# Optimization experiments

Measured on AMD Instinct MI355X. Metric: run time of the kernel, lower is better.

## Reference

```python
import jax, jax.numpy as jnp
import numpy as np

EPS = 1e-5  # torch LayerNorm default


def setup_inputs() -> dict:
    key = jax.random.key(0)
    ks = jax.random.split(key, 4)
    B, S, D = 8, 1024, 768
    return {
        "q": jax.random.normal(ks[0], (B, S, D), dtype=jnp.float32),
        "k": jax.random.normal(ks[1], (B, S, D), dtype=jnp.float32),
        "v": jax.random.normal(ks[2], (B, S, D), dtype=jnp.float32),
        "W": jax.random.normal(ks[3], (D, D), dtype=jnp.float32) * (1.0 / np.sqrt(D)),
        "gamma": jnp.ones((D,), dtype=jnp.float32),
        "beta": jnp.zeros((D,), dtype=jnp.float32),
        "n_heads": 12,
    }


def reference(q, k, v, W, gamma, beta, n_heads):
    # Shapes: q,k,v [B,S,D]; W [D,D] (torch Linear weight, y = x @ W.T)
    B, S, D = q.shape
    Dh = D // n_heads

    proj = lambda x: jax.nn.relu(x @ W.T)
    q1, k1, v1 = proj(q), proj(k), proj(v)

    # chunk(dim=2) + cat(dim=0) == reshape to per-head [B,S,H,Dh]
    split = lambda x: x.reshape(B, S, n_heads, Dh)
    qh, kh, vh = split(q1), split(k1), split(v1)

    scale = 1.0 / (Dh ** 0.5)
    scores = jnp.einsum("bqhd,bkhd->bhqk", qh, kh) * scale  # [B,H,S,S]
    attn = jax.nn.softmax(scores, axis=-1)  # dropout is identity in eval mode
    out = jnp.einsum("bhqk,bkhd->bqhd", attn, vh).reshape(B, S, D)

    # `outputs += outputs + q` in torch -> outputs = 2*outputs + q
    out = 2.0 * out + q

    mu = jnp.mean(out, axis=-1, keepdims=True)
    var = jnp.var(out, axis=-1, keepdims=True)
    return (out - mu) / jnp.sqrt(var + EPS) * gamma + beta
```

## Files before the change

### kernel.cpp

```cpp
#include <hip/hip_runtime.h>
#include <hip/hip_bf16.h>

#define B_  8
#define S_  1024
#define D_  768
#define H_  12
#define DH_ 64

typedef __attribute__((ext_vector_type(8))) short bf16x8;
typedef __attribute__((ext_vector_type(4))) float f32x4;
typedef __attribute__((ext_vector_type(16))) float f32x16;

__device__ inline short f2bf(float f) {
    unsigned u = __builtin_bit_cast(unsigned, f);
    u = (u + 0x7fffu + ((u >> 16) & 1u)) >> 16;
    return (short)u;
}
__device__ inline float exp2_fast(float x) {
    float r; asm("v_exp_f32 %0, %1" : "=v"(r) : "v"(x)); return r;
}
__device__ inline unsigned cvt_pk_bf16(float lo, float hi) {
    unsigned r; asm("v_cvt_pk_bf16_f32 %0, %1, %2" : "=v"(r) : "v"(lo), "v"(hi)); return r;
}
__device__ inline float rcp_fast(float x) {
    float r; asm("v_rcp_f32 %0, %1" : "=v"(r) : "v"(x)); return r;
}
__device__ inline void plswap(unsigned& a, unsigned& b) {
    auto r = __builtin_amdgcn_permlane32_swap(a, b, false, false);
    a = r[0]; b = r[1];
}
__device__ inline float2 xhalves(float x) {
    unsigned u = __builtin_bit_cast(unsigned, x);
    auto r = __builtin_amdgcn_permlane32_swap(u, u, false, false);
    return make_float2(__builtin_bit_cast(float, r[0]),
                       __builtin_bit_cast(float, r[1]));
}

__global__ __launch_bounds__(256) void proj_kernel(
    const float* __restrict__ q, const float* __restrict__ k,
    const float* __restrict__ v, const float* __restrict__ W,
    short* __restrict__ q1, short* __restrict__ k1, short* __restrict__ v1t)
{
    __shared__ __align__(16) char lds_raw[32768];

    int p  = blockIdx.x;
    int L  = (p & 7) * 144 + (p >> 3);
    int mt = L / 6, nt = L % 6;
    int t  = mt >> 6;
    int m0 = (mt & 63) << 7;
    int n0 = nt << 7;
    const float* X = (t == 0) ? q : (t == 1) ? k : v;

    int tid = threadIdx.x, lane = tid & 63, w = tid >> 6;
    int wr = w >> 1, wc = w & 1;
    int l15 = lane & 15, g = lane >> 4;

    int srow = tid >> 1, h = tid & 1;
    const float* ax = X + (size_t)(m0 + srow) * D_ + h * 16;
    const float* bx = W + (size_t)(n0 + srow) * D_ + h * 16;

    int wb0 = srow * 64 + ((((h << 1) | 0) ^ (srow & 3)) << 4);
    int wb1 = srow * 64 + ((((h << 1) | 1) ^ (srow & 3)) << 4);
    int fs = (g ^ (l15 & 3)) << 4;

    f32x4 la[4], lb[4];
#define LOADAB(step) do { int _c = (step) * 32; \
        la[0] = *(const f32x4*)(ax + _c);      la[1] = *(const f32x4*)(ax + _c + 4); \
        la[2] = *(const f32x4*)(ax + _c + 8);  la[3] = *(const f32x4*)(ax + _c + 12); \
        lb[0] = *(const f32x4*)(bx + _c);      lb[1] = *(const f32x4*)(bx + _c + 4); \
        lb[2] = *(const f32x4*)(bx + _c + 8);  lb[3] = *(const f32x4*)(bx + _c + 12); \
    } while (0)
#define CONVW(bufbase) do { \
        uint4 ua0, ua1, ub0, ub1; \
        ua0.x = cvt_pk_bf16(la[0][0], la[0][1]); ua0.y = cvt_pk_bf16(la[0][2], la[0][3]); \
        ua0.z = cvt_pk_bf16(la[1][0], la[1][1]); ua0.w = cvt_pk_bf16(la[1][2], la[1][3]); \
        ua1.x = cvt_pk_bf16(la[2][0], la[2][1]); ua1.y = cvt_pk_bf16(la[2][2], la[2][3]); \
        ua1.z = cvt_pk_bf16(la[3][0], la[3][1]); ua1.w = cvt_pk_bf16(la[3][2], la[3][3]); \
        ub0.x = cvt_pk_bf16(lb[0][0], lb[0][1]); ub0.y = cvt_pk_bf16(lb[0][2], lb[0][3]); \
        ub0.z = cvt_pk_bf16(lb[1][0], lb[1][1]); ub0.w = cvt_pk_bf16(lb[1][2], lb[1][3]); \
        ub1.x = cvt_pk_bf16(lb[2][0], lb[2][1]); ub1.y = cvt_pk_bf16(lb[2][2], lb[2][3]); \
        ub1.z = cvt_pk_bf16(lb[3][0], lb[3][1]); ub1.w = cvt_pk_bf16(lb[3][2], lb[3][3]); \
        *(uint4*)(lds_raw + (bufbase) + wb0)        = ua0; \
        *(uint4*)(lds_raw + (bufbase) + wb1)        = ua1; \
        *(uint4*)(lds_raw + (bufbase) + 8192 + wb0) = ub0; \
        *(uint4*)(lds_raw + (bufbase) + 8192 + wb1) = ub1; \
    } while (0)

    f32x4 acc[4][4];
    #pragma unroll
    for (int m = 0; m < 4; m++)
        #pragma unroll
        for (int n = 0; n < 4; n++) acc[m][n] = (f32x4){0.f, 0.f, 0.f, 0.f};

    LOADAB(0);
    CONVW(0);
    LOADAB(1);
    asm volatile("s_waitcnt lgkmcnt(0)" ::: "memory");
    __builtin_amdgcn_s_barrier();
    asm volatile("" ::: "memory");

    #pragma unroll 2
    for (int s = 0; s < 24; ++s) {
        if (s < 23) CONVW(((s + 1) & 1) << 14);
        if (s < 22) LOADAB(s + 2);
        const char* bufp = lds_raw + ((s & 1) << 14);
        bf16x8 af[4], bfv[4];
        #pragma unroll
        for (int m = 0; m < 4; m++)
            af[m] = *(const bf16x8*)(bufp + (wr * 64 + m * 16 + l15) * 64 + fs);
        #pragma unroll
        for (int n = 0; n < 4; n++)
            bfv[n] = *(const bf16x8*)(bufp + 8192 + (wc * 64 + n * 16 + l15) * 64 + fs);
        __builtin_amdgcn_s_setprio(1);
        #pragma unroll
        for (int m = 0; m < 4; m++)
            #pragma unroll
            for (int n = 0; n < 4; n++)
                acc[m][n] = __builtin_amdgcn_mfma_f32_16x16x32_bf16(
                    af[m], bfv[n], acc[m][n], 0, 0, 0);
        __builtin_amdgcn_s_setprio(0);
        if (s < 23) {
            asm volatile("s_waitcnt lgkmcnt(0)" ::: "memory");
            __builtin_amdgcn_s_barrier();
            asm volatile("" ::: "memory");
        }
    }
#undef LOADAB
#undef CONVW

    __syncthreads();
    const float sc1 = (t == 1) ? 0.18033688011112793f : 1.0f;
    #pragma unroll
    for (int m = 0; m < 4; m++) {
        int rb = wr * 64 + m * 16 + (g << 2);
        #pragma unroll
        for (int n = 0; n < 4; n++) {
            int cb = wc * 64 + n * 16 + l15;
            #pragma unroll
            for (int r = 0; r < 4; r++) {
                short vv = f2bf(fmaxf(acc[m][n][r], 0.f) * sc1);
                int rr = (t == 2) ? cb : rb + r;
                int cc = (t == 2) ? rb + r : cb;
                *(short*)(lds_raw + rr * 256 + (((cc >> 3) ^ (rr & 15)) << 4)
                          + ((cc & 7) << 1)) = vv;
            }
        }
    }
    __syncthreads();
    int row = tid >> 1;
    int c0  = (tid & 1) << 6;
    bf16x8 ov[8];
    #pragma unroll
    for (int j = 0; j < 8; j++)
        ov[j] = *(const bf16x8*)(lds_raw + row * 256 +
                 ((((c0 >> 3) + j) ^ (row & 15)) << 4));
    if (t == 2) {
        int gc = n0 + row;
        int hh2 = gc >> 6, dh = gc & 63;
        int bb = m0 >> 10, s0 = m0 & 1023;
        short* dst = v1t + (((size_t)bb * H_ + hh2) * DH_ + dh) * S_ + s0 + c0;
        #pragma unroll
        for (int j = 0; j < 8; j++) *(bf16x8*)(dst + j * 8) = ov[j];
    } else {
        int m = m0 + row;
        int bb = m >> 10, ss = m & 1023;
        int hh2 = (n0 >> 6) + (tid & 1);
        short* dst = (t ? k1 : q1) + (((size_t)bb * H_ + hh2) * S_ + ss) * DH_;
        #pragma unroll
        for (int j = 0; j < 8; j++) *(bf16x8*)(dst + j * 8) = ov[j];
    }
}

__global__ __launch_bounds__(256, 3) void attn_kernel(
    const short* __restrict__ q1, const short* __restrict__ k1,
    const short* __restrict__ v1t, float* __restrict__ out)
{
    __shared__ short Klds[2][4096];
    __shared__ short Vlds[2][4096];
    __shared__ float lsum_lds[4][32];

    int d    = blockIdx.x;
    int head = (d & 7) + ((d >> 6) << 3);
    int qi   = (d >> 3) & 7;
    int bb   = head / H_, hh = head % H_;

    int tid = threadIdx.x, lane = tid & 63, w = tid >> 6;
    int l31 = lane & 31, hi = lane >> 5;
    int qbase = (qi * 4 + w) * 32;

    const short* Qp = q1  + (size_t)head * S_ * DH_;
    const short* Kp = k1  + (size_t)head * S_ * DH_;
    const short* Vp = v1t + (size_t)head * DH_ * S_;

    int sr = tid >> 2, sc = tid & 3;
    int swz0 = sr * 128 + ((sc       ^ (sr & 7)) << 4);
    int swz1 = sr * 128 + (((sc + 4) ^ (sr & 7)) << 4);

    bf16x8 stK0, stK1, stV0, stV1;

#define LOADST(kvb) do { \
        const short* _kg = Kp + (size_t)((kvb) + sr) * DH_; \
        const short* _vg = Vp + (size_t)sr * S_ + (kvb); \
        stK0 = *(const bf16x8*)(_kg + sc * 8); \
        stK1 = *(const bf16x8*)(_kg + (sc + 4) * 8); \
        stV0 = *(const bf16x8*)(_vg + sc * 8); \
        stV1 = *(const bf16x8*)(_vg + (sc + 4) * 8); \
    } while (0)
#define WRITEST(buf) do { \
        char* _kb = (char*)&Klds[buf][0]; \
        char* _vb = (char*)&Vlds[buf][0]; \
        *(bf16x8*)(_kb + swz0) = stK0; \
        *(bf16x8*)(_kb + swz1) = stK1; \
        *(bf16x8*)(_vb + swz0) = stV0; \
        *(bf16x8*)(_vb + swz1) = stV1; \
    } while (0)

    bf16x8 qf[4];
    #pragma unroll
    for (int kb = 0; kb < 4; kb++)
        qf[kb] = *(const bf16x8*)(Qp + (size_t)(qbase + l31) * DH_ + kb * 16 + hi * 8);

    f32x16 o0, o1;
    #pragma unroll
    for (int r = 0; r < 16; r++) { o0[r] = 0.f; o1[r] = 0.f; }
    float mreg = -1e30f, lsum = 0.f;

    int xk = l31 & 7;

    auto subtile = [&](int cur, int j) {
        const char* Kt = (const char*)&Klds[cur][0];
        const char* Vt = (const char*)&Vlds[cur][0];
        int rK = (32 * j + l31) * 128;
        bf16x8 kf0 = *(const bf16x8*)(Kt + rK + (((0 + hi) ^ xk) << 4));
        bf16x8 kf1 = *(const bf16x8*)(Kt + rK + (((2 + hi) ^ xk) << 4));
        bf16x8 kf2 = *(const bf16x8*)(Kt + rK + (((4 + hi) ^ xk) << 4));
        bf16x8 kf3 = *(const bf16x8*)(Kt + rK + (((6 + hi) ^ xk) << 4));
        int rV0 = l31 * 128, rV1 = (32 + l31) * 128;
        int s0 = ((4 * j + hi) ^ xk) << 4, s1 = ((4 * j + 2 + hi) ^ xk) << 4;
        bf16x8 vf00 = *(const bf16x8*)(Vt + rV0 + s0);
        bf16x8 vf01 = *(const bf16x8*)(Vt + rV0 + s1);
        bf16x8 vf10 = *(const bf16x8*)(Vt + rV1 + s0);
        bf16x8 vf11 = *(const bf16x8*)(Vt + rV1 + s1);

        f32x16 s;
        #pragma unroll
        for (int r = 0; r < 16; r++) s[r] = 0.f;
        __builtin_amdgcn_s_setprio(1);
        s = __builtin_amdgcn_mfma_f32_32x32x16_bf16(kf0, qf[0], s, 0, 0, 0);
        s = __builtin_amdgcn_mfma_f32_32x32x16_bf16(kf1, qf[1], s, 0, 0, 0);
        s = __builtin_amdgcn_mfma_f32_32x32x16_bf16(kf2, qf[2], s, 0, 0, 0);
        s = __builtin_amdgcn_mfma_f32_32x32x16_bf16(kf3, qf[3], s, 0, 0, 0);
        __builtin_amdgcn_s_setprio(0);

        float t0 = fmaxf(s[0], s[1]),   t1 = fmaxf(s[2], s[3]);
        float t2 = fmaxf(s[4], s[5]),   t3 = fmaxf(s[6], s[7]);
        float t4 = fmaxf(s[8], s[9]),   t5 = fmaxf(s[10], s[11]);
        float t6 = fmaxf(s[12], s[13]), t7 = fmaxf(s[14], s[15]);
        float u0 = fmaxf(t0, t1), u1 = fmaxf(t2, t3);
        float u2 = fmaxf(t4, t5), u3 = fmaxf(t6, t7);
        float pmax = fmaxf(fmaxf(u0, u1), fmaxf(u2, u3));
        float2 ph = xhalves(pmax);
        pmax = fmaxf(ph.x, ph.y);

        if (!__all(pmax <= mreg + 8.f)) {
            float mn = fmaxf(mreg, pmax);
            float sc_ = exp2_fast(mreg - mn);
            mreg = mn; lsum *= sc_;
            if (hi == 0) lsum_lds[w][l31] = sc_;
            asm volatile("s_waitcnt lgkmcnt(0)" ::: "memory");
            #pragma unroll
            for (int r = 0; r < 16; r++) {
                int crow = (r & 3) + ((r >> 2) << 3) + (hi << 2);
                float srw = lsum_lds[w][crow];
                o0[r] *= srw; o1[r] *= srw;
            }
        }

        #pragma unroll
        for (int r = 0; r < 16; r++) s[r] = exp2_fast(s[r] - mreg);

        float a0 = s[0] + s[1],   a1 = s[2] + s[3];
        float a2 = s[4] + s[5],   a3 = s[6] + s[7];
        float a4 = s[8] + s[9],   a5 = s[10] + s[11];
        float a6 = s[12] + s[13], a7 = s[14] + s[15];
        float rsum = ((a0 + a1) + (a2 + a3)) + ((a4 + a5) + (a6 + a7));
        float2 rh = xhalves(rsum);
        lsum += rh.x + rh.y;

        unsigned c0 = cvt_pk_bf16(s[0], s[1]);
        unsigned c1 = cvt_pk_bf16(s[2], s[3]);
        unsigned c2 = cvt_pk_bf16(s[4], s[5]);
        unsigned c3 = cvt_pk_bf16(s[6], s[7]);
        unsigned c4 = cvt_pk_bf16(s[8], s[9]);
        unsigned c5 = cvt_pk_bf16(s[10], s[11]);
        unsigned c6 = cvt_pk_bf16(s[12], s[13]);
        unsigned c7 = cvt_pk_bf16(s[14], s[15]);
        plswap(c0, c2);
        plswap(c1, c3);
        plswap(c4, c6);
        plswap(c5, c7);

        union U { unsigned u[4]; bf16x8 v; };
        U f0, f1;
        f0.u[0] = c0; f0.u[1] = c1; f0.u[2] = c2; f0.u[3] = c3;
        f1.u[0] = c4; f1.u[1] = c5; f1.u[2] = c6; f1.u[3] = c7;

        __builtin_amdgcn_s_setprio(1);
        o0 = __builtin_amdgcn_mfma_f32_32x32x16_bf16(f0.v, vf00, o0, 0, 0, 0);
        o0 = __builtin_amdgcn_mfma_f32_32x32x16_bf16(f1.v, vf01, o0, 0, 0, 0);
        o1 = __builtin_amdgcn_mfma_f32_32x32x16_bf16(f0.v, vf10, o1, 0, 0, 0);
        o1 = __builtin_amdgcn_mfma_f32_32x32x16_bf16(f1.v, vf11, o1, 0, 0, 0);
        __builtin_amdgcn_s_setprio(0);
    };

    LOADST(0);
    WRITEST(0);
    LOADST(64);
    asm volatile("s_waitcnt lgkmcnt(0)" ::: "memory");
    __builtin_amdgcn_s_barrier();
    asm volatile("" ::: "memory");

    int cur = 0;
    for (int t = 0; t < 16; t++) {
        if (t < 15) {
            WRITEST(cur ^ 1);
            if (t < 14) LOADST((t + 2) * 64);
        }
        subtile(cur, 0);
        subtile(cur, 1);
        if (t < 15) {
            asm volatile("" ::: "memory");
            asm volatile("s_waitcnt lgkmcnt(0)" ::: "memory");
            __builtin_amdgcn_s_barrier();
            asm volatile("" ::: "memory");
        }
        cur ^= 1;
    }
#undef LOADST
#undef WRITEST

    if (hi == 0) lsum_lds[w][l31] = lsum;
    asm volatile("s_waitcnt lgkmcnt(0)" ::: "memory");
    #pragma unroll
    for (int r = 0; r < 16; r++) {
        int crow = (r & 3) + ((r >> 2) << 3) + (hi << 2);
        float inv = rcp_fast(lsum_lds[w][crow]);
        float* op = out + ((size_t)(bb * S_ + qbase + crow)) * D_ + hh * DH_ + l31;
        op[0]  = o0[r] * inv;
        op[32] = o1[r] * inv;
    }
}

__global__ __launch_bounds__(192) void ln_kernel(
    const float* __restrict__ qin, const float* __restrict__ gamma,
    const float* __restrict__ beta, float* __restrict__ out)
{
    int row = blockIdx.x;
    int tid = threadIdx.x;
    size_t base = (size_t)row * D_ + tid * 4;

    f32x4 o  = *(const f32x4*)(out + base);
    f32x4 qv = *(const f32x4*)(qin + base);
    f32x4 x;
    float sum = 0.f, sq = 0.f;
    #pragma unroll
    for (int i = 0; i < 4; i++) {
        x[i] = 2.f * o[i] + qv[i];
        sum += x[i];
        sq  += x[i] * x[i];
    }
    #pragma unroll
    for (int msk = 1; msk < 64; msk <<= 1) {
        sum += __shfl_xor(sum, msk);
        sq  += __shfl_xor(sq, msk);
    }
    __shared__ float s1[3], s2[3];
    if ((tid & 63) == 0) { s1[tid >> 6] = sum; s2[tid >> 6] = sq; }
    __syncthreads();
    sum = s1[0] + s1[1] + s1[2];
    sq  = s2[0] + s2[1] + s2[2];
    float mu   = sum * (1.f / D_);
    float var  = sq * (1.f / D_) - mu * mu;
    float rstd = rsqrtf(var + 1e-5f);
    f32x4 g = *(const f32x4*)(gamma + tid * 4);
    f32x4 b = *(const f32x4*)(beta + tid * 4);
    f32x4 y;
    #pragma unroll
    for (int i = 0; i < 4; i++)
        y[i] = (x[i] - mu) * rstd * g[i] + b[i];
    *(f32x4*)(out + base) = y;
}

extern "C" void kernel_launch(void* const* d_in, const int* in_sizes, int n_in,
                              void* d_out, int out_size, void* d_ws, size_t ws_size,
                              hipStream_t stream)
{
    const float* q     = (const float*)d_in[0];
    const float* k     = (const float*)d_in[1];
    const float* v     = (const float*)d_in[2];
    const float* W     = (const float*)d_in[3];
    const float* gamma = (const float*)d_in[4];
    const float* beta  = (const float*)d_in[5];

    size_t per = (size_t)B_ * H_ * S_ * DH_;
    short* q1  = (short*)d_ws;
    short* k1  = q1 + per;
    short* v1t = k1 + per;
    float* out = (float*)d_out;

    proj_kernel<<<dim3(1152), dim3(256), 0, stream>>>(q, k, v, W, q1, k1, v1t);
    attn_kernel<<<dim3(768), dim3(256), 0, stream>>>(q1, k1, v1t, out);
    ln_kernel<<<dim3(B_ * S_), dim3(192), 0, stream>>>(q, gamma, beta, out);
}
```

Measured before the change: 130.2 us.

## Load projection GEMM tiles directly into LDS with global_load_lds

Result: no change. 128.0 us (-1.7%).

```diff
diff --git a/kernel.cpp b/kernel.cpp
--- a/kernel.cpp
+++ b/kernel.cpp
@@ -34,6 +34,12 @@
     auto r = __builtin_amdgcn_permlane32_swap(u, u, false, false);
     return make_float2(__builtin_bit_cast(float, r[0]),
                        __builtin_bit_cast(float, r[1]));
+}
+__device__ inline void gl_lds16(const float* gsrc, char* ldst) {
+    __builtin_amdgcn_global_load_lds(
+        (const __attribute__((address_space(1))) unsigned int*)gsrc,
+        (__attribute__((address_space(3))) unsigned int*)ldst,
+        16, 0, 0);
 }
 
 __global__ __launch_bounds__(256) void proj_kernel(
@@ -55,36 +61,15 @@
     int wr = w >> 1, wc = w & 1;
     int l15 = lane & 15, g = lane >> 4;
 
-    int srow = tid >> 1, h = tid & 1;
-    const float* ax = X + (size_t)(m0 + srow) * D_ + h * 16;
-    const float* bx = W + (size_t)(n0 + srow) * D_ + h * 16;
-
-    int wb0 = srow * 64 + ((((h << 1) | 0) ^ (srow & 3)) << 4);
-    int wb1 = srow * 64 + ((((h << 1) | 1) ^ (srow & 3)) << 4);
-    int fs = (g ^ (l15 & 3)) << 4;
-
-    f32x4 la[4], lb[4];
-#define LOADAB(step) do { int _c = (step) * 32; \
-        la[0] = *(const f32x4*)(ax + _c);      la[1] = *(const f32x4*)(ax + _c + 4); \
-        la[2] = *(const f32x4*)(ax + _c + 8);  la[3] = *(const f32x4*)(ax + _c + 12); \
-        lb[0] = *(const f32x4*)(bx + _c);      lb[1] = *(const f32x4*)(bx + _c + 4); \
-        lb[2] = *(const f32x4*)(bx + _c + 8);  lb[3] = *(const f32x4*)(bx + _c + 12); \
-    } while (0)
-#define CONVW(bufbase) do { \
-        uint4 ua0, ua1, ub0, ub1; \
-        ua0.x = cvt_pk_bf16(la[0][0], la[0][1]); ua0.y = cvt_pk_bf16(la[0][2], la[0][3]); \
-        ua0.z = cvt_pk_bf16(la[1][0], la[1][1]); ua0.w = cvt_pk_bf16(la[1][2], la[1][3]); \
-        ua1.x = cvt_pk_bf16(la[2][0], la[2][1]); ua1.y = cvt_pk_bf16(la[2][2], la[2][3]); \
-        ua1.z = cvt_pk_bf16(la[3][0], la[3][1]); ua1.w = cvt_pk_bf16(la[3][2], la[3][3]); \
-        ub0.x = cvt_pk_bf16(lb[0][0], lb[0][1]); ub0.y = cvt_pk_bf16(lb[0][2], lb[0][3]); \
-        ub0.z = cvt_pk_bf16(lb[1][0], lb[1][1]); ub0.w = cvt_pk_bf16(lb[1][2], lb[1][3]); \
-        ub1.x = cvt_pk_bf16(lb[2][0], lb[2][1]); ub1.y = cvt_pk_bf16(lb[2][2], lb[2][3]); \
-        ub1.z = cvt_pk_bf16(lb[3][0], lb[3][1]); ub1.w = cvt_pk_bf16(lb[3][2], lb[3][3]); \
-        *(uint4*)(lds_raw + (bufbase) + wb0)        = ua0; \
-        *(uint4*)(lds_raw + (bufbase) + wb1)        = ua1; \
-        *(uint4*)(lds_raw + (bufbase) + 8192 + wb0) = ub0; \
-        *(uint4*)(lds_raw + (bufbase) + 8192 + wb1) = ub1; \
-    } while (0)
+    const float* srcA[4];
+    const float* srcB[4];
+    #pragma unroll
+    for (int i = 0; i < 4; i++) {
+        int r  = w * 32 + i * 8 + (lane >> 3);
+        int sp = (lane & 7) ^ (r & 7);
+        srcA[i] = X + (size_t)(m0 + r) * D_ + sp * 4;
+        srcB[i] = W + (size_t)(n0 + r) * D_ + sp * 4;
+    }
 
     f32x4 acc[4][4];
     #pragma unroll
@@ -92,25 +77,41 @@
         #pragma unroll
         for (int n = 0; n < 4; n++) acc[m][n] = (f32x4){0.f, 0.f, 0.f, 0.f};
 
-    LOADAB(0);
-    CONVW(0);
-    LOADAB(1);
-    asm volatile("s_waitcnt lgkmcnt(0)" ::: "memory");
-    __builtin_amdgcn_s_barrier();
-    asm volatile("" ::: "memory");
-
-    #pragma unroll 2
-    for (int s = 0; s < 24; ++s) {
-        if (s < 23) CONVW(((s + 1) & 1) << 14);
-        if (s < 22) LOADAB(s + 2);
-        const char* bufp = lds_raw + ((s & 1) << 14);
+    for (int kb = 0; kb < 24; ++kb) {
+        __builtin_amdgcn_s_barrier();
+        asm volatile("" ::: "memory");
+        #pragma unroll
+        for (int i = 0; i < 4; i++) {
+            gl_lds16(srcA[i] + kb * 32, lds_raw + w * 4096 + i * 1024);
+            gl_lds16(srcB[i] + kb * 32, lds_raw + 16384 + w * 4096 + i * 1024);
+        }
+        asm volatile("s_waitcnt vmcnt(0)" ::: "memory");
+        __builtin_amdgcn_s_barrier();
+        asm volatile("" ::: "memory");
+
         bf16x8 af[4], bfv[4];
         #pragma unroll
-        for (int m = 0; m < 4; m++)
-            af[m] = *(const bf16x8*)(bufp + (wr * 64 + m * 16 + l15) * 64 + fs);
-        #pragma unroll
-        for (int n = 0; n < 4; n++)
-            bfv[n] = *(const bf16x8*)(bufp + 8192 + (wc * 64 + n * 16 + l15) * 64 + fs);
+        for (int m = 0; m < 4; m++) {
+            int r = wr * 64 + m * 16 + l15;
+            const char* rp = lds_raw + r * 128;
+            f32x4 lo = *(const f32x4*)(rp + (((2 * g)     ^ (r & 7)) << 4));
+            f32x4 hi = *(const f32x4*)(rp + (((2 * g + 1) ^ (r & 7)) << 4));
+            uint4 pk;
+            pk.x = cvt_pk_bf16(lo[0], lo[1]); pk.y = cvt_pk_bf16(lo[2], lo[3]);
+            pk.z = cvt_pk_bf16(hi[0], hi[1]); pk.w = cvt_pk_bf16(hi[2], hi[3]);
+            af[m] = __builtin_bit_cast(bf16x8, pk);
+        }
+        #pragma unroll
+        for (int n = 0; n < 4; n++) {
+            int r = wc * 64 + n * 16 + l15;
+            const char* rp = lds_raw + 16384 + r * 128;
+            f32x4 lo = *(const f32x4*)(rp + (((2 * g)     ^ (r & 7)) << 4));
+            f32x4 hi = *(const f32x4*)(rp + (((2 * g + 1) ^ (r & 7)) << 4));
+            uint4 pk;
+            pk.x = cvt_pk_bf16(lo[0], lo[1]); pk.y = cvt_pk_bf16(lo[2], lo[3]);
+            pk.z = cvt_pk_bf16(hi[0], hi[1]); pk.w = cvt_pk_bf16(hi[2], hi[3]);
+            bfv[n] = __builtin_bit_cast(bf16x8, pk);
+        }
         __builtin_amdgcn_s_setprio(1);
         #pragma unroll
         for (int m = 0; m < 4; m++)
@@ -119,14 +120,7 @@
                 acc[m][n] = __builtin_amdgcn_mfma_f32_16x16x32_bf16(
                     af[m], bfv[n], acc[m][n], 0, 0, 0);
         __builtin_amdgcn_s_setprio(0);
-        if (s < 23) {
-            asm volatile("s_waitcnt lgkmcnt(0)" ::: "memory");
-            __builtin_amdgcn_s_barrier();
-            asm volatile("" ::: "memory");
-        }
-    }
-#undef LOADAB
-#undef CONVW
+    }
 
     __syncthreads();
     const float sc1 = (t == 1) ? 0.18033688011112793f : 1.0f;
```
